# Performance work log

Measured on AMD Instinct MI355X. Metric: run time of the kernel, lower is better.

The kernel has to match this reference:

```python
import jax, jax.numpy as jnp
import numpy as np

ORDER = 25
L = ORDER + 1
K = 64
B = 262144
N_ITER = 8
WEIGHT_FLOOR = 1e-05
VAR_FLOOR = 1e-06
LOG_PI = L * float(np.log(2.0 * np.pi))  # (order+1)*log(2*pi)


def setup_inputs() -> dict:
    key = jax.random.key(0)
    k1, k2 = jax.random.split(key)
    x = jax.random.normal(k1, (B, L), dtype=jnp.float32)
    mu0 = jax.random.normal(k2, (K, L), dtype=jnp.float32)      # torch.randn(K, L)
    w0 = jnp.ones((K,), dtype=jnp.float32)                      # normalized to 1/K in reference
    sigma0 = jnp.ones((K, L), dtype=jnp.float32)                # diagonal of eye(L)
    return {"x": x, "w0": w0, "mu0": mu0, "sigma0": sigma0}


def _em_step(x, w, mu, sig):
    # ---- E-step (diag covariance path of the torch module) ----
    log_det = jnp.sum(jnp.log(sig), axis=-1)                    # [K]
    prec = 1.0 / sig                                            # [K,L]
    # mahala[b,k] = sum_l (x[b,l]-mu[k,l])^2 * prec[k,l]
    # expanded quadratic form to avoid materializing [B,K,L]
    mahala = ((x * x) @ prec.T
              - 2.0 * (x @ (mu * prec).T)
              + jnp.sum(mu * mu * prec, axis=-1))               # [B,K]
    numer = jnp.log(w) - 0.5 * (LOG_PI + log_det + mahala)      # [B,K]
    denom = jax.scipy.special.logsumexp(numer, axis=-1, keepdims=True)
    posterior = jnp.exp(numer - denom)                          # [B,K]
    ll = jnp.sum(denom)
    # ---- M-step (alpha == 0) ----
    z = jnp.sum(posterior, axis=0)                              # [K]
    w_new = z / B
    zinv = 1.0 / z
    # weight flooring + renormalization
    w_new = jnp.maximum(w_new, WEIGHT_FLOOR)
    sum_floor = WEIGHT_FLOOR * K
    a = (1.0 - sum_floor) / (jnp.sum(w_new) - sum_floor)
    b = WEIGHT_FLOOR * (1.0 - a)
    w_new = a * w_new + b
    px = posterior.T @ x                                        # [K,L]
    mu_new = px * zinv[:, None]
    pxx = posterior.T @ (x * x)                                 # [K,L]
    sig_new = pxx * zinv[:, None] - mu_new * mu_new
    sig_new = jnp.maximum(sig_new, VAR_FLOOR)                   # variance flooring
    return w_new, mu_new, sig_new, ll


def reference(x, w0, mu0, sigma0):
    w = w0 / jnp.sum(w0)                                        # == 1/K for ones init

    def body(carry, _):
        w, mu, sig, _ = carry
        w, mu, sig, ll = _em_step(x, w, mu, sig)
        return (w, mu, sig, ll), None

    init = (w, mu0, sigma0, jnp.zeros((), dtype=jnp.float32))
    (w, mu, sig, ll), _ = jax.lax.scan(body, init, None, length=N_ITER)
    sigma = jax.vmap(jnp.diag)(sig)                             # [K,L,L] diagonal covariances
    return w, mu, sigma, ll
```

## Files before the change

kernel.cpp:

```cpp
#include <hip/hip_runtime.h>
#include <math.h>

typedef _Float16 f16x8 __attribute__((ext_vector_type(8)));
typedef float f32x16 __attribute__((ext_vector_type(16)));
typedef unsigned int uint4v __attribute__((ext_vector_type(4)));

namespace {
constexpr int LDIM = 26;
constexpr int KDIM = 64;
constexpr int NSAMP = 262144;
constexpr int NITER = 8;
constexpr float WFLOOR = 1e-5f;
constexpr float VFLOOR = 1e-6f;
constexpr float LOG2PI_TERM = 47.784803726642976f;
constexpr float L2E = 1.44269504088896340736f;
constexpr float LN2 = 0.69314718055994530942f;

constexpr int ACC_STRIDE = 53;
constexpr int ACC_N = KDIM * ACC_STRIDE + 1;
constexpr int NCOPIES = 8;
constexpr int WROW = 36;
constexpr int NBLK = 1024;
constexpr int PART_STRIDE = 3408;
}

__device__ float g_partial[NBLK * PART_STRIDE];
__device__ float g_accum[NCOPIES * ACC_N];
__device__ float g_w[KDIM];
__device__ float g_mu[KDIM * LDIM];
__device__ float g_sig[KDIM * LDIM];
__device__ float g_ll[1];
__device__ __align__(16) unsigned g_coef[KDIM * WROW];

__device__ __forceinline__ unsigned pkrtz(float a, float b) {
  return __builtin_bit_cast(unsigned, __builtin_amdgcn_cvt_pkrtz(a, b));
}
__device__ __forceinline__ f16x8 ld8h(const unsigned* p) {
  uint4v v = *(const uint4v*)p;
  return __builtin_bit_cast(f16x8, v);
}
__device__ __forceinline__ f32x16 mfma16(f16x8 a, f16x8 b, f32x16 c) {
  return __builtin_amdgcn_mfma_f32_32x32x16_f16(a, b, c, 0, 0, 0);
}
__device__ __forceinline__ void gload16(const void* g, void* l) {
  __builtin_amdgcn_global_load_lds(
      (const __attribute__((address_space(1))) unsigned*)g,
      (__attribute__((address_space(3))) unsigned*)l, 16, 0, 0);
}

__device__ void pack_row(int k, float w, const float* mu, const float* sg, unsigned* wp) {
  float A[LDIM], Bv[LDIM];
  float logdet = 0.f, q = 0.f;
#pragma unroll
  for (int l = 0; l < LDIM; ++l) {
    float pr = 1.0f / sg[l];
    logdet += __logf(sg[l]);
    A[l] = -0.5f * pr;
    Bv[l] = mu[l] * pr;
    q = __builtin_fmaf(mu[l] * mu[l], pr, q);
  }
  float C = __logf(w) - 0.5f * (LOG2PI_TERM + logdet + q);
  float Chi = (float)__builtin_amdgcn_cvt_pkrtz(C, 0.0f)[0];
  float Clo = C - Chi;
  unsigned* row = wp + k * WROW;
#define CF(f) ((f) < 26 ? A[(f)] : (f) < 52 ? Bv[(f) - 26] : (f) == 52 ? C : (f) == 53 ? Clo : 0.0f)
#pragma unroll
  for (int D = 0; D < 32; ++D) row[D] = pkrtz(CF(2 * D), CF(2 * D + 1));
#undef CF
#pragma unroll
  for (int D = 32; D < 36; ++D) row[D] = 0u;
}

__global__ void prep_coef(const float* __restrict__ w0, const float* __restrict__ mu0,
                          const float* __restrict__ sig0) {
  const int k = threadIdx.x;
  float wv = w0[k];
  float s = wv;
#pragma unroll
  for (int d = 1; d < 64; d <<= 1) s += __shfl_xor(s, d, 64);
  float w = wv / s;
  float mu[LDIM], sg[LDIM];
#pragma unroll
  for (int l = 0; l < LDIM; ++l) {
    mu[l] = mu0[k * LDIM + l];
    sg[l] = sig0[k * LDIM + l];
  }
  pack_row(k, w, mu, sg, g_coef);
}

__global__ __launch_bounds__(128, 2) void em_mfma(const float* __restrict__ x) {
  __shared__ __align__(16) unsigned char pool[16384];
  __shared__ __align__(16) float stage[2][2][32 * LDIM];

  const int tid = threadIdx.x;
  const int lane = tid & 63;
  const int warp = tid >> 6;
  const int sl = lane & 31;
  const int h = lane >> 5;

  unsigned short* XTs = (unsigned short*)&pool[warp * 4096];
  unsigned short* SQs = (unsigned short*)&pool[warp * 4096 + 2048];
  unsigned short* PT0s = (unsigned short*)&pool[8192 + warp * 4096];
  unsigned short* PT1s = (unsigned short*)&pool[8192 + warp * 4096 + 2048];
  const unsigned* XTd = (const unsigned*)XTs;
  const unsigned* SQd = (const unsigned*)SQs;
  const unsigned* PT0d = (const unsigned*)PT0s;
  const unsigned* PT1d = (const unsigned*)PT1s;

  f32x16 aX0 = {0,0,0,0,0,0,0,0,0,0,0,0,0,0,0,0};
  f32x16 aX1 = {0,0,0,0,0,0,0,0,0,0,0,0,0,0,0,0};
  f32x16 aQ0 = {0,0,0,0,0,0,0,0,0,0,0,0,0,0,0,0};
  f32x16 aQ1 = {0,0,0,0,0,0,0,0,0,0,0,0,0,0,0,0};
  float llacc = 0.f;

  const int sbase = blockIdx.x * 256 + warp * 128;
  const int rowbase0 = sl * WROW;
  const int rowbase1 = (32 + sl) * WROW;

  f16x8 ca00 = ld8h(g_coef + rowbase0 + 0 + 4 * h);
  f16x8 ca01 = ld8h(g_coef + rowbase0 + 8 + 4 * h);
  f16x8 ca02 = ld8h(g_coef + rowbase0 + 16 + 4 * h);
  f16x8 ca03 = ld8h(g_coef + rowbase0 + 24 + 4 * h);
  f16x8 ca10 = ld8h(g_coef + rowbase1 + 0 + 4 * h);
  f16x8 ca11 = ld8h(g_coef + rowbase1 + 8 + 4 * h);
  f16x8 ca12 = ld8h(g_coef + rowbase1 + 16 + 4 * h);
  f16x8 ca13 = ld8h(g_coef + rowbase1 + 24 + 4 * h);

  auto stage_tile = [&](int tt) {
    const uint4v* tb = (const uint4v*)(x + (size_t)(sbase + 32 * tt) * LDIM);
    char* db = (char*)&stage[warp][tt & 1][0];
    gload16(tb + lane, db + (size_t)lane * 16);
    gload16(tb + 64 + lane, db + 1024 + (size_t)lane * 16);
    gload16(tb + 128 + lane, db + 2048 + (size_t)lane * 16);
    if (lane < 16) gload16(tb + 192 + lane, db + 3072 + (size_t)lane * 16);
  };

  stage_tile(0);

#pragma unroll
  for (int t = 0; t < 4; ++t) {
    asm volatile("s_waitcnt vmcnt(0)" ::: "memory");

    unsigned xhu[13], squ[13];
    {
      const float2* srow = (const float2*)&stage[warp][t & 1][sl * LDIM];
#pragma unroll
      for (int j = 0; j < 13; ++j) {
        float2 v = srow[j];
        xhu[j] = pkrtz(v.x, v.y);
        squ[j] = pkrtz(v.x * v.x, v.y * v.y);
      }
    }

    if (t < 3) stage_tile(t + 1);

    {
      unsigned short* Ts = h ? SQs : XTs;
#pragma unroll
      for (int c = 0; c < LDIM; ++c) {
        unsigned src = h ? squ[c >> 1] : xhu[c >> 1];
        unsigned v = (c & 1) ? (src >> 16) : (src & 0xffffu);
        Ts[(c * 32 + sl) ^ ((c & 7) << 3)] = (unsigned short)v;
      }
      Ts[(26 * 32 + sl) ^ ((26 & 7) << 3)] = h ? (unsigned short)0 : (unsigned short)0x3C00;
    }

    f32x16 e0 = {0,0,0,0,0,0,0,0,0,0,0,0,0,0,0,0};
    f32x16 e1 = {0,0,0,0,0,0,0,0,0,0,0,0,0,0,0,0};
    {
      uint4v b0 = {h ? squ[4] : squ[0], h ? squ[5] : squ[1],
                   h ? squ[6] : squ[2], h ? squ[7] : squ[3]};
      uint4v b1 = {h ? squ[12] : squ[8], h ? xhu[0] : squ[9],
                   h ? xhu[1] : squ[10], h ? xhu[2] : squ[11]};
      uint4v b2 = {h ? xhu[7] : xhu[3], h ? xhu[8] : xhu[4],
                   h ? xhu[9] : xhu[5], h ? xhu[10] : xhu[6]};
      uint4v b3 = {h ? 0u : xhu[11], h ? 0u : xhu[12],
                   h ? 0u : 0x3C003C00u, 0u};
      f16x8 fb0 = __builtin_bit_cast(f16x8, b0);
      f16x8 fb1 = __builtin_bit_cast(f16x8, b1);
      f16x8 fb2 = __builtin_bit_cast(f16x8, b2);
      f16x8 fb3 = __builtin_bit_cast(f16x8, b3);
      e0 = mfma16(ca00, fb0, e0);
      e1 = mfma16(ca10, fb0, e1);
      e0 = mfma16(ca01, fb1, e0);
      e1 = mfma16(ca11, fb1, e1);
      e0 = mfma16(ca02, fb2, e0);
      e1 = mfma16(ca12, fb2, e1);
      e0 = mfma16(ca03, fb3, e0);
      e1 = mfma16(ca13, fb3, e1);
    }

    float m8[8];
#pragma unroll
    for (int r = 0; r < 8; ++r)
      m8[r] = fmaxf(fmaxf(e0[r], e0[r + 8]), fmaxf(e1[r], e1[r + 8]));
#pragma unroll
    for (int d = 4; d > 0; d >>= 1)
#pragma unroll
      for (int r = 0; r < d; ++r) m8[r] = fmaxf(m8[r], m8[r + d]);
    const float M = fmaxf(m8[0], __shfl_xor(m8[0], 32));
    const float mL = M * L2E;
#pragma unroll
    for (int r = 0; r < 16; ++r) {
      e0[r] = __builtin_amdgcn_exp2f(__builtin_fmaf(e0[r], L2E, -mL));
      e1[r] = __builtin_amdgcn_exp2f(__builtin_fmaf(e1[r], L2E, -mL));
    }
    float s8[8];
#pragma unroll
    for (int r = 0; r < 8; ++r)
      s8[r] = (e0[r] + e0[r + 8]) + (e1[r] + e1[r + 8]);
#pragma unroll
    for (int d = 4; d > 0; d >>= 1)
#pragma unroll
      for (int r = 0; r < d; ++r) s8[r] += s8[r + d];
    const float SS = s8[0] + __shfl_xor(s8[0], 32);
    const float scale = __builtin_amdgcn_rcpf(SS);
    llacc += M + __builtin_amdgcn_logf(SS) * LN2;

#pragma unroll
    for (int r = 0; r < 16; ++r) {
      const int row = (r & 3) + 8 * (r >> 2) + 4 * h;
      const int idx = (row * 32 + sl) ^ ((row & 7) << 3);
      _Float16 p0 = (_Float16)(e0[r] * scale);
      _Float16 p1 = (_Float16)(e1[r] * scale);
      PT0s[idx] = __builtin_bit_cast(unsigned short, p0);
      PT1s[idx] = __builtin_bit_cast(unsigned short, p1);
    }

#pragma unroll
    for (int ks = 0; ks < 2; ++ks) {
      const int off = 8 * ks + 4 * h;
      const int swz = (sl & 7) << 2;
      f16x8 a0 = ld8h(&PT0d[(sl * 16 + off) ^ swz]);
      f16x8 a1 = ld8h(&PT1d[(sl * 16 + off) ^ swz]);
      f16x8 bx = ld8h(&XTd[(sl * 16 + off) ^ swz]);
      f16x8 bq = ld8h(&SQd[(sl * 16 + off) ^ swz]);
      aX0 = mfma16(a0, bx, aX0);
      aQ0 = mfma16(a0, bq, aQ0);
      aX1 = mfma16(a1, bx, aX1);
      aQ1 = mfma16(a1, bq, aQ1);
    }
  }

  __syncthreads();
  float* red = (float*)&pool[0];
  float llw = llacc * 0.5f;
#pragma unroll
  for (int d = 1; d < 64; d <<= 1) llw += __shfl_xor(llw, d, 64);
  if (warp == 0) {
#pragma unroll
    for (int r = 0; r < 16; ++r) {
      const int row = (r & 3) + 8 * (r >> 2) + 4 * h;
      if (sl < 26) {
        red[row * ACC_STRIDE + 1 + sl] = aX0[r];
        red[row * ACC_STRIDE + 27 + sl] = aQ0[r];
        red[(row + 32) * ACC_STRIDE + 1 + sl] = aX1[r];
        red[(row + 32) * ACC_STRIDE + 27 + sl] = aQ1[r];
      } else if (sl == 26) {
        red[row * ACC_STRIDE] = aX0[r];
        red[(row + 32) * ACC_STRIDE] = aX1[r];
      }
    }
    if (lane == 0) red[KDIM * ACC_STRIDE] = llw;
  }
  __syncthreads();
  if (warp == 1) {
    float* pb = g_partial + (size_t)blockIdx.x * PART_STRIDE;
#pragma unroll
    for (int r = 0; r < 16; ++r) {
      const int row = (r & 3) + 8 * (r >> 2) + 4 * h;
      if (sl < 26) {
        pb[row * ACC_STRIDE + 1 + sl] = red[row * ACC_STRIDE + 1 + sl] + aX0[r];
        pb[row * ACC_STRIDE + 27 + sl] = red[row * ACC_STRIDE + 27 + sl] + aQ0[r];
        pb[(row + 32) * ACC_STRIDE + 1 + sl] = red[(row + 32) * ACC_STRIDE + 1 + sl] + aX1[r];
        pb[(row + 32) * ACC_STRIDE + 27 + sl] = red[(row + 32) * ACC_STRIDE + 27 + sl] + aQ1[r];
      } else if (sl == 26) {
        pb[row * ACC_STRIDE] = red[row * ACC_STRIDE] + aX0[r];
        pb[(row + 32) * ACC_STRIDE] = red[(row + 32) * ACC_STRIDE] + aX1[r];
      }
    }
    if (lane == 0) pb[KDIM * ACC_STRIDE] = red[KDIM * ACC_STRIDE] + llw;
  }
}

__global__ void reduce_partials() {
  const int i = blockIdx.x * 256 + threadIdx.x;
  if (i >= ACC_N) return;
  const int cy = blockIdx.y;
  const float* p = g_partial + (size_t)cy * 128 * PART_STRIDE + i;
  float s = 0.f;
#pragma unroll 8
  for (int j = 0; j < 128; ++j) s += p[(size_t)j * PART_STRIDE];
  g_accum[cy * ACC_N + i] = s;
}

__global__ void finalize_k() {
  const int k = threadIdx.x;
  float vals[ACC_STRIDE];
#pragma unroll
  for (int j = 0; j < ACC_STRIDE; ++j) vals[j] = 0.f;
  float llsum = 0.f;
  for (int cp = 0; cp < NCOPIES; ++cp) {
    const float* a = g_accum + cp * ACC_N;
#pragma unroll
    for (int j = 0; j < ACC_STRIDE; ++j) vals[j] += a[k * ACC_STRIDE + j];
    llsum += a[KDIM * ACC_STRIDE];
  }
  float z = vals[0];
  float wn = z * (1.0f / NSAMP);
  float wf = fmaxf(wn, WFLOOR);
  float S = wf;
#pragma unroll
  for (int d = 1; d < 64; d <<= 1) S += __shfl_xor(S, d, 64);
  const float sf = WFLOOR * KDIM;
  float a = (1.0f - sf) / (S - sf);
  float b = WFLOOR * (1.0f - a);
  float w = a * wf + b;
  g_w[k] = w;
  float zinv = 1.0f / z;
  float muk[LDIM], sgk[LDIM];
#pragma unroll
  for (int l = 0; l < LDIM; ++l) {
    float m = vals[1 + l] * zinv;
    float s2 = fmaxf(__builtin_fmaf(-m, m, vals[27 + l] * zinv), VFLOOR);
    muk[l] = m;
    sgk[l] = s2;
    g_mu[k * LDIM + l] = m;
    g_sig[k * LDIM + l] = s2;
  }
  if (k == 0) g_ll[0] = llsum;
  pack_row(k, w, muk, sgk, g_coef);
}

__global__ void writeout(float* __restrict__ out) {
  const int i = blockIdx.x * 256 + threadIdx.x;
  if (i < 64) {
    out[i] = g_w[i];
  } else if (i < 64 + KDIM * LDIM) {
    out[i] = g_mu[i - 64];
  } else if (i < 64 + KDIM * LDIM + KDIM * LDIM * LDIM) {
    int t = i - (64 + KDIM * LDIM);
    int k = t / (LDIM * LDIM);
    int r = t % (LDIM * LDIM);
    int ii = r / LDIM;
    int jj = r % LDIM;
    out[i] = (ii == jj) ? g_sig[k * LDIM + ii] : 0.f;
  } else if (i == 64 + KDIM * LDIM + KDIM * LDIM * LDIM) {
    out[i] = g_ll[0];
  }
}

extern "C" void kernel_launch(void* const* d_in, const int* in_sizes, int n_in,
                              void* d_out, int out_size, void* d_ws, size_t ws_size,
                              hipStream_t stream) {
  (void)in_sizes; (void)n_in; (void)d_ws; (void)ws_size; (void)out_size;
  const float* x   = (const float*)d_in[0];
  const float* w0  = (const float*)d_in[1];
  const float* mu0 = (const float*)d_in[2];
  const float* sg0 = (const float*)d_in[3];
  float* out = (float*)d_out;

  prep_coef<<<1, 64, 0, stream>>>(w0, mu0, sg0);
  for (int it = 0; it < NITER; ++it) {
    em_mfma<<<NBLK, 128, 0, stream>>>(x);
    reduce_partials<<<dim3(14, 8), 256, 0, stream>>>();
    finalize_k<<<1, 64, 0, stream>>>();
  }
  const int nout = 64 + KDIM * LDIM + KDIM * LDIM * LDIM + 1;
  writeout<<<(nout + 255) / 256, 256, 0, stream>>>(out);
}
```

Measured before the change: 301.5 us.

## Prepack x into fp16 MFMA fragments once and reuse across EM iterations

Adds a pack_x kernel that runs once per call and converts x into fp16 B-fragments plus swizzled transposed x/x² LDS images in global scratch. The 8 EM iterations then stream these prepacked images directly instead of re-converting fp32 x every iteration. This removes per-iteration conversion, transpose and LDS writes, and halves bytes read per iteration (fp16 vs fp32). The cost is one extra packing pass and 64 MB of extra global scratch buffers. The transformed input is rebuilt on every call, so nothing carries across calls.

After: 318.5 us. 1.06x slower.

```diff
diff --git a/kernel.cpp b/kernel.cpp
--- a/kernel.cpp
+++ b/kernel.cpp
@@ -21,6 +21,7 @@
 constexpr int NCOPIES = 8;
 constexpr int WROW = 36;
 constexpr int NBLK = 1024;
+constexpr int NTILE = NSAMP / 32;
 constexpr int PART_STRIDE = 3408;
 }
 
@@ -31,6 +32,8 @@
 __device__ float g_sig[KDIM * LDIM];
 __device__ float g_ll[1];
 __device__ __align__(16) unsigned g_coef[KDIM * WROW];
+__device__ __align__(16) unsigned g_xtimg[NTILE * 1024];
+__device__ __align__(16) unsigned g_bfrag[NTILE * 1024];
 
 __device__ __forceinline__ unsigned pkrtz(float a, float b) {
   return __builtin_bit_cast(unsigned, __builtin_amdgcn_cvt_pkrtz(a, b));
@@ -88,9 +91,71 @@
   pack_row(k, w, mu, sg, g_coef);
 }
 
+__global__ void pack_x(const float* __restrict__ x) {
+  const int tile = blockIdx.x;
+  const int tid = threadIdx.x;
+  const int sl = tid & 31;
+  const int half = tid >> 5;
+  __shared__ __align__(16) unsigned short img[2048];
+
+  {
+    uint4v z = {0, 0, 0, 0};
+    uint4v* ip = (uint4v*)img;
+#pragma unroll
+    for (int i = 0; i < 4; ++i) ip[tid + 64 * i] = z;
+  }
+  __syncthreads();
+
+  unsigned xhu[13], squ[13];
+  {
+    const float2* xp = (const float2*)(x + (size_t)(tile * 32 + sl) * LDIM);
+#pragma unroll
+    for (int j = 0; j < 13; ++j) {
+      float2 v = xp[j];
+      xhu[j] = pkrtz(v.x, v.y);
+      squ[j] = pkrtz(v.x * v.x, v.y * v.y);
+    }
+  }
+
+  {
+    unsigned short* Ts = img + half * 1024;
+#pragma unroll
+    for (int c = 0; c < LDIM; ++c) {
+      unsigned src = half ? squ[c >> 1] : xhu[c >> 1];
+      unsigned v = (c & 1) ? (src >> 16) : (src & 0xffffu);
+      Ts[(c * 32 + sl) ^ ((c & 7) << 3)] = (unsigned short)v;
+    }
+    Ts[(26 * 32 + sl) ^ ((26 & 7) << 3)] = half ? (unsigned short)0 : (unsigned short)0x3C00;
+  }
+
+  {
+    uint4v b0 = {half ? squ[4] : squ[0], half ? squ[5] : squ[1],
+                 half ? squ[6] : squ[2], half ? squ[7] : squ[3]};
+    uint4v b1 = {half ? squ[12] : squ[8], half ? xhu[0] : squ[9],
+                 half ? xhu[1] : squ[10], half ? xhu[2] : squ[11]};
+    uint4v b2 = {half ? xhu[7] : xhu[3], half ? xhu[8] : xhu[4],
+                 half ? xhu[9] : xhu[5], half ? xhu[10] : xhu[6]};
+    uint4v b3 = {half ? 0u : xhu[11], half ? 0u : xhu[12],
+                 half ? 0u : 0x3C003C00u, 0u};
+    uint4v* bp = (uint4v*)g_bfrag + (size_t)tile * 256;
+    bp[0 * 64 + half * 32 + sl] = b0;
+    bp[1 * 64 + half * 32 + sl] = b1;
+    bp[2 * 64 + half * 32 + sl] = b2;
+    bp[3 * 64 + half * 32 + sl] = b3;
+  }
+  __syncthreads();
+
+  {
+    const uint4v* ip = (const uint4v*)img;
+    uint4v* op = (uint4v*)g_xtimg + (size_t)tile * 256;
+#pragma unroll
+    for (int i = 0; i < 4; ++i) op[tid + 64 * i] = ip[tid + 64 * i];
+  }
+}
+
 __global__ __launch_bounds__(128, 2) void em_mfma(const float* __restrict__ x) {
-  __shared__ __align__(16) unsigned char pool[16384];
-  __shared__ __align__(16) float stage[2][2][32 * LDIM];
+  (void)x;
+  __shared__ __align__(16) unsigned char pool[2][12288];
 
   const int tid = threadIdx.x;
   const int lane = tid & 63;
@@ -98,12 +163,8 @@
   const int sl = lane & 31;
   const int h = lane >> 5;
 
-  unsigned short* XTs = (unsigned short*)&pool[warp * 4096];
-  unsigned short* SQs = (unsigned short*)&pool[warp * 4096 + 2048];
-  unsigned short* PT0s = (unsigned short*)&pool[8192 + warp * 4096];
-  unsigned short* PT1s = (unsigned short*)&pool[8192 + warp * 4096 + 2048];
-  const unsigned* XTd = (const unsigned*)XTs;
-  const unsigned* SQd = (const unsigned*)SQs;
+  unsigned short* PT0s = (unsigned short*)&pool[warp][0];
+  unsigned short* PT1s = (unsigned short*)&pool[warp][2048];
   const unsigned* PT0d = (const unsigned*)PT0s;
   const unsigned* PT1d = (const unsigned*)PT1s;
 
@@ -113,7 +174,7 @@
   f32x16 aQ1 = {0,0,0,0,0,0,0,0,0,0,0,0,0,0,0,0};
   float llacc = 0.f;
 
-  const int sbase = blockIdx.x * 256 + warp * 128;
+  const int tbase = blockIdx.x * 8 + warp * 4;
   const int rowbase0 = sl * WROW;
   const int rowbase1 = (32 + sl) * WROW;
 
@@ -126,60 +187,45 @@
   f16x8 ca12 = ld8h(g_coef + rowbase1 + 16 + 4 * h);
   f16x8 ca13 = ld8h(g_coef + rowbase1 + 24 + 4 * h);
 
-  auto stage_tile = [&](int tt) {
-    const uint4v* tb = (const uint4v*)(x + (size_t)(sbase + 32 * tt) * LDIM);
-    char* db = (char*)&stage[warp][tt & 1][0];
-    gload16(tb + lane, db + (size_t)lane * 16);
-    gload16(tb + 64 + lane, db + 1024 + (size_t)lane * 16);
-    gload16(tb + 128 + lane, db + 2048 + (size_t)lane * 16);
-    if (lane < 16) gload16(tb + 192 + lane, db + 3072 + (size_t)lane * 16);
-  };
-
-  stage_tile(0);
+  uint4v bf[2][4];
+
+  {
+    const uint4v* bt = (const uint4v*)g_bfrag + (size_t)tbase * 256;
+    bf[0][0] = bt[0 * 64 + lane];
+    bf[0][1] = bt[1 * 64 + lane];
+    bf[0][2] = bt[2 * 64 + lane];
+    bf[0][3] = bt[3 * 64 + lane];
+    const uint4v* it = (const uint4v*)g_xtimg + (size_t)tbase * 256;
+    char* db = (char*)&pool[warp][4096];
+#pragma unroll
+    for (int i = 0; i < 4; ++i)
+      gload16(it + i * 64 + lane, db + i * 1024 + (size_t)lane * 16);
+  }
 
 #pragma unroll
   for (int t = 0; t < 4; ++t) {
     asm volatile("s_waitcnt vmcnt(0)" ::: "memory");
 
-    unsigned xhu[13], squ[13];
-    {
-      const float2* srow = (const float2*)&stage[warp][t & 1][sl * LDIM];
-#pragma unroll
-      for (int j = 0; j < 13; ++j) {
-        float2 v = srow[j];
-        xhu[j] = pkrtz(v.x, v.y);
-        squ[j] = pkrtz(v.x * v.x, v.y * v.y);
-      }
-    }
-
-    if (t < 3) stage_tile(t + 1);
-
-    {
-      unsigned short* Ts = h ? SQs : XTs;
-#pragma unroll
-      for (int c = 0; c < LDIM; ++c) {
-        unsigned src = h ? squ[c >> 1] : xhu[c >> 1];
-        unsigned v = (c & 1) ? (src >> 16) : (src & 0xffffu);
-        Ts[(c * 32 + sl) ^ ((c & 7) << 3)] = (unsigned short)v;
-      }
-      Ts[(26 * 32 + sl) ^ ((26 & 7) << 3)] = h ? (unsigned short)0 : (unsigned short)0x3C00;
+    if (t < 3) {
+      const uint4v* bt = (const uint4v*)g_bfrag + (size_t)(tbase + t + 1) * 256;
+      bf[(t + 1) & 1][0] = bt[0 * 64 + lane];
+      bf[(t + 1) & 1][1] = bt[1 * 64 + lane];
+      bf[(t + 1) & 1][2] = bt[2 * 64 + lane];
+      bf[(t + 1) & 1][3] = bt[3 * 64 + lane];
+      const uint4v* it = (const uint4v*)g_xtimg + (size_t)(tbase + t + 1) * 256;
+      char* db = (char*)&pool[warp][4096 + ((t + 1) & 1) * 4096];
+#pragma unroll
+      for (int i = 0; i < 4; ++i)
+        gload16(it + i * 64 + lane, db + i * 1024 + (size_t)lane * 16);
     }
 
     f32x16 e0 = {0,0,0,0,0,0,0,0,0,0,0,0,0,0,0,0};
     f32x16 e1 = {0,0,0,0,0,0,0,0,0,0,0,0,0,0,0,0};
     {
-      uint4v b0 = {h ? squ[4] : squ[0], h ? squ[5] : squ[1],
-                   h ? squ[6] : squ[2], h ? squ[7] : squ[3]};
-      uint4v b1 = {h ? squ[12] : squ[8], h ? xhu[0] : squ[9],
-                   h ? xhu[1] : squ[10], h ? xhu[2] : squ[11]};
-      uint4v b2 = {h ? xhu[7] : xhu[3], h ? xhu[8] : xhu[4],
-                   h ? xhu[9] : xhu[5], h ? xhu[10] : xhu[6]};
-      uint4v b3 = {h ? 0u : xhu[11], h ? 0u : xhu[12],
-                   h ? 0u : 0x3C003C00u, 0u};
-      f16x8 fb0 = __builtin_bit_cast(f16x8, b0);
-      f16x8 fb1 = __builtin_bit_cast(f16x8, b1);
-      f16x8 fb2 = __builtin_bit_cast(f16x8, b2);
-      f16x8 fb3 = __builtin_bit_cast(f16x8, b3);
+      f16x8 fb0 = __builtin_bit_cast(f16x8, bf[t & 1][0]);
+      f16x8 fb1 = __builtin_bit_cast(f16x8, bf[t & 1][1]);
+      f16x8 fb2 = __builtin_bit_cast(f16x8, bf[t & 1][2]);
+      f16x8 fb3 = __builtin_bit_cast(f16x8, bf[t & 1][3]);
       e0 = mfma16(ca00, fb0, e0);
       e1 = mfma16(ca10, fb0, e1);
       e0 = mfma16(ca01, fb1, e0);
@@ -227,6 +273,8 @@
       PT1s[idx] = __builtin_bit_cast(unsigned short, p1);
     }
 
+    const unsigned* XTd = (const unsigned*)&pool[warp][4096 + (t & 1) * 4096];
+    const unsigned* SQd = XTd + 512;
 #pragma unroll
     for (int ks = 0; ks < 2; ++ks) {
       const int off = 8 * ks + 4 * h;
@@ -243,7 +291,7 @@
   }
 
   __syncthreads();
-  float* red = (float*)&pool[0];
+  float* red = (float*)&pool[0][0];
   float llw = llacc * 0.5f;
 #pragma unroll
   for (int d = 1; d < 64; d <<= 1) llw += __shfl_xor(llw, d, 64);
@@ -361,6 +409,7 @@
   float* out = (float*)d_out;
 
   prep_coef<<<1, 64, 0, stream>>>(w0, mu0, sg0);
+  pack_x<<<NTILE, 64, 0, stream>>>(x);
   for (int it = 0; it < NITER; ++it) {
     em_mfma<<<NBLK, 128, 0, stream>>>(x);
     reduce_partials<<<dim3(14, 8), 256, 0, stream>>>();
```

## Pre-pack x to fp16 once and stream compact rows in EM kernel

Applied to the files above, without the earlier changes.

A new pack16 kernel converts x to fp16 pairs once, padded to 16 words per sample, so the eight EM iterations each read half the bytes instead of fp32 rows. The squares are now computed in fp16 from the rounded values rather than from fp32, which changes precision slightly. The grid is doubled to 2048 blocks with fewer tiles per block, occupancy is raised to 4 blocks per SM, and the partial reduction is widened to match. It adds a one-time pack pass and a larger partial buffer.

Measured after the change: 418.7 us. 38.9% more time.

```diff
diff --git a/kernel.cpp b/kernel.cpp
--- a/kernel.cpp
+++ b/kernel.cpp
@@ -1,6 +1,7 @@
 #include <hip/hip_runtime.h>
 #include <math.h>
 
+typedef _Float16 f16x2 __attribute__((ext_vector_type(2)));
 typedef _Float16 f16x8 __attribute__((ext_vector_type(8)));
 typedef float f32x16 __attribute__((ext_vector_type(16)));
 typedef unsigned int uint4v __attribute__((ext_vector_type(4)));
@@ -20,7 +21,7 @@
 constexpr int ACC_N = KDIM * ACC_STRIDE + 1;
 constexpr int NCOPIES = 8;
 constexpr int WROW = 36;
-constexpr int NBLK = 1024;
+constexpr int NBLK = 2048;
 constexpr int PART_STRIDE = 3408;
 }
 
@@ -31,9 +32,15 @@
 __device__ float g_sig[KDIM * LDIM];
 __device__ float g_ll[1];
 __device__ __align__(16) unsigned g_coef[KDIM * WROW];
+__device__ __align__(16) unsigned g_x16[NSAMP * 16];
 
 __device__ __forceinline__ unsigned pkrtz(float a, float b) {
   return __builtin_bit_cast(unsigned, __builtin_amdgcn_cvt_pkrtz(a, b));
+}
+__device__ __forceinline__ unsigned sqr16(unsigned u) {
+  f16x2 a = __builtin_bit_cast(f16x2, u);
+  a = a * a;
+  return __builtin_bit_cast(unsigned, a);
 }
 __device__ __forceinline__ f16x8 ld8h(const unsigned* p) {
   uint4v v = *(const uint4v*)p;
@@ -88,9 +95,22 @@
   pack_row(k, w, mu, sg, g_coef);
 }
 
-__global__ __launch_bounds__(128, 2) void em_mfma(const float* __restrict__ x) {
+__global__ void pack16(const float* __restrict__ x) {
+  const int total = NSAMP * 16;
+  for (int idx = blockIdx.x * 256 + threadIdx.x; idx < total; idx += gridDim.x * 256) {
+    const int s = idx >> 4, j = idx & 15;
+    unsigned v = 0u;
+    if (j < 13) {
+      float2 p = *(const float2*)(x + (size_t)s * LDIM + 2 * j);
+      v = pkrtz(p.x, p.y);
+    }
+    g_x16[idx] = v;
+  }
+}
+
+__global__ __launch_bounds__(128, 4) void em_mfma() {
   __shared__ __align__(16) unsigned char pool[16384];
-  __shared__ __align__(16) float stage[2][2][32 * LDIM];
+  __shared__ __align__(16) unsigned stage[2][2][512];
 
   const int tid = threadIdx.x;
   const int lane = tid & 63;
@@ -113,7 +133,7 @@
   f32x16 aQ1 = {0,0,0,0,0,0,0,0,0,0,0,0,0,0,0,0};
   float llacc = 0.f;
 
-  const int sbase = blockIdx.x * 256 + warp * 128;
+  const int sbase = blockIdx.x * 128 + warp * 64;
   const int rowbase0 = sl * WROW;
   const int rowbase1 = (32 + sl) * WROW;
 
@@ -127,32 +147,34 @@
   f16x8 ca13 = ld8h(g_coef + rowbase1 + 24 + 4 * h);
 
   auto stage_tile = [&](int tt) {
-    const uint4v* tb = (const uint4v*)(x + (size_t)(sbase + 32 * tt) * LDIM);
+    const uint4v* tb = (const uint4v*)(g_x16 + (size_t)(sbase + 32 * tt) * 16);
     char* db = (char*)&stage[warp][tt & 1][0];
     gload16(tb + lane, db + (size_t)lane * 16);
     gload16(tb + 64 + lane, db + 1024 + (size_t)lane * 16);
-    gload16(tb + 128 + lane, db + 2048 + (size_t)lane * 16);
-    if (lane < 16) gload16(tb + 192 + lane, db + 3072 + (size_t)lane * 16);
   };
 
   stage_tile(0);
 
 #pragma unroll
-  for (int t = 0; t < 4; ++t) {
+  for (int t = 0; t < 2; ++t) {
     asm volatile("s_waitcnt vmcnt(0)" ::: "memory");
 
     unsigned xhu[13], squ[13];
     {
-      const float2* srow = (const float2*)&stage[warp][t & 1][sl * LDIM];
-#pragma unroll
-      for (int j = 0; j < 13; ++j) {
-        float2 v = srow[j];
-        xhu[j] = pkrtz(v.x, v.y);
-        squ[j] = pkrtz(v.x * v.x, v.y * v.y);
-      }
-    }
-
-    if (t < 3) stage_tile(t + 1);
+      const unsigned* srow = &stage[warp][t & 1][sl * 16];
+      uint4v r0 = *(const uint4v*)(srow);
+      uint4v r1 = *(const uint4v*)(srow + 4);
+      uint4v r2 = *(const uint4v*)(srow + 8);
+      unsigned r12 = srow[12];
+      xhu[0] = r0[0]; xhu[1] = r0[1]; xhu[2] = r0[2]; xhu[3] = r0[3];
+      xhu[4] = r1[0]; xhu[5] = r1[1]; xhu[6] = r1[2]; xhu[7] = r1[3];
+      xhu[8] = r2[0]; xhu[9] = r2[1]; xhu[10] = r2[2]; xhu[11] = r2[3];
+      xhu[12] = r12;
+#pragma unroll
+      for (int j = 0; j < 13; ++j) squ[j] = sqr16(xhu[j]);
+    }
+
+    if (t < 1) stage_tile(t + 1);
 
     {
       unsigned short* Ts = h ? SQs : XTs;
@@ -287,10 +309,10 @@
   const int i = blockIdx.x * 256 + threadIdx.x;
   if (i >= ACC_N) return;
   const int cy = blockIdx.y;
-  const float* p = g_partial + (size_t)cy * 128 * PART_STRIDE + i;
+  const float* p = g_partial + (size_t)cy * 256 * PART_STRIDE + i;
   float s = 0.f;
 #pragma unroll 8
-  for (int j = 0; j < 128; ++j) s += p[(size_t)j * PART_STRIDE];
+  for (int j = 0; j < 256; ++j) s += p[(size_t)j * PART_STRIDE];
   g_accum[cy * ACC_N + i] = s;
 }
 
@@ -361,8 +383,9 @@
   float* out = (float*)d_out;
 
   prep_coef<<<1, 64, 0, stream>>>(w0, mu0, sg0);
+  pack16<<<2048, 256, 0, stream>>>(x);
   for (int it = 0; it < NITER; ++it) {
-    em_mfma<<<NBLK, 128, 0, stream>>>(x);
+    em_mfma<<<NBLK, 128, 0, stream>>>();
     reduce_partials<<<dim3(14, 8), 256, 0, stream>>>();
     finalize_k<<<1, 64, 0, stream>>>();
   }
```
